# Optimization experiments

Hardware: AMD Instinct MI355X
Metric: run time of the kernel (lower is better)

## Reference

```python
import jax, jax.numpy as jnp
import numpy as np

B, N, C, H = 1, 4096, 512, 8
S = 64  # sqrt(N), static


def setup_inputs() -> dict:
    key = jax.random.key(0)
    ks = jax.random.split(key, 4)
    d = C // H
    return {
        "x": jax.random.normal(ks[0], (B, N, C), dtype=jnp.float32),
        "num_heads": H,
        "bias": jnp.zeros((1,), dtype=jnp.float32),  # unused in original forward
        "scale": jnp.asarray(d ** -0.5, dtype=jnp.float32),
        "Wqkv": jax.random.normal(ks[1], (3 * C, C), dtype=jnp.float32) * (C ** -0.5),
        "bqkv": jnp.zeros((3 * C,), dtype=jnp.float32),
        "Wproj": jax.random.normal(ks[2], (C, C), dtype=jnp.float32) * (C ** -0.5),
        "bproj": jnp.zeros((C,), dtype=jnp.float32),
    }


def reference(x, num_heads, bias, scale, Wqkv, bqkv, Wproj, bproj):
    b, n, c = x.shape
    d = c // num_heads
    # fused QKV projection: [b, n, 3c] -> [3, b, h, n, d]
    qkv = (x @ Wqkv.T + bqkv).reshape(b, n, 3, num_heads, d).transpose(2, 0, 3, 1, 4)
    q, k, v = qkv[0] * scale, qkv[1], qkv[2]
    attn = jax.nn.softmax(jnp.einsum("bhnd,bhmd->bhnm", q, k), axis=-1)
    out = jnp.einsum("bhnm,bhmd->bhnd", attn, v)
    out = out.transpose(0, 2, 1, 3).reshape(b, n, c)
    out = out @ Wproj.T + bproj
    return out.reshape(b, S, S, c)
```

## Files before the change

### kernel.cpp

```cpp
#include <hip/hip_runtime.h>
#include <stdint.h>

#define NTOK 4096
#define CDIM 512
#define HEADS 8
#define DHEAD 64
#define PHEAD (NTOK * DHEAD)

typedef __bf16 bf16x8 __attribute__((ext_vector_type(8)));
typedef float f32x4 __attribute__((ext_vector_type(4)));

typedef const __attribute__((address_space(1))) unsigned int* gas_ptr;
typedef __attribute__((address_space(3))) unsigned int* las_ptr;

__device__ __forceinline__ unsigned short bfbits(float f) {
    return __builtin_bit_cast(unsigned short, (__bf16)f);
}

__device__ __forceinline__ f32x4 mfma32(bf16x8 a, bf16x8 b, f32x4 c) {
    return __builtin_amdgcn_mfma_f32_16x16x32_bf16(a, b, c, 0, 0, 0);
}

__device__ __forceinline__ void gload16(const unsigned short* g, unsigned short* l) {
    __builtin_amdgcn_global_load_lds((gas_ptr)g, (las_ptr)l, 16, 0, 0);
}

__device__ __forceinline__ void cvt_store8(unsigned short* dst, float4 v0, float4 v1) {
    unsigned short o[8];
    o[0] = bfbits(v0.x); o[1] = bfbits(v0.y); o[2] = bfbits(v0.z); o[3] = bfbits(v0.w);
    o[4] = bfbits(v1.x); o[5] = bfbits(v1.y); o[6] = bfbits(v1.z); o[7] = bfbits(v1.w);
    *(uint4*)dst = *(const uint4*)o;
}

__global__ __launch_bounds__(256) void cast3_k(
    const float* __restrict__ x, const float* __restrict__ wq, const float* __restrict__ wp,
    unsigned short* __restrict__ xb, unsigned short* __restrict__ wqb,
    unsigned short* __restrict__ wpb)
{
    const int b = blockIdx.x;
    const float* src; unsigned short* dst; int off;
    if (b < 1024)      { src = x;  dst = xb;  off = b; }
    else if (b < 1408) { src = wq; dst = wqb; off = b - 1024; }
    else               { src = wp; dst = wpb; off = b - 1408; }
    const int i = (off * 256 + threadIdx.x) * 8;
    const float4 v0 = *(const float4*)(src + i);
    const float4 v1 = *(const float4*)(src + i + 4);
    cvt_store8(dst + i, v0, v1);
}

__global__ __launch_bounds__(256) void gemm_qkv(
    const unsigned short* __restrict__ A,
    const unsigned short* __restrict__ Bm,
    const float* __restrict__ bias,
    const float* __restrict__ scale_p,
    unsigned short* __restrict__ qkv_out)
{
    __shared__ __align__(16) unsigned short smem[64 * 136];
    unsigned short* lA = smem;
    unsigned short* lB = smem + 2048;

    const int tid = threadIdx.x;
    const int mBase = blockIdx.y * 64, nBase = blockIdx.x * 128;
    const int lane = tid & 63;
    const int w = __builtin_amdgcn_readfirstlane(tid >> 6);
    const int l16 = lane & 15, quad = lane >> 4;

    const unsigned short* gA  = &A[(size_t)(mBase + (tid >> 2)) * CDIM + (tid & 3) * 8];
    const unsigned short* gB0 = &Bm[(size_t)(nBase + (tid >> 2)) * CDIM + (tid & 3) * 8];
    const unsigned short* gB1 = &Bm[(size_t)(nBase + 64 + (tid >> 2)) * CDIM + (tid & 3) * 8];
    unsigned short* sA  = &lA[tid * 8];
    unsigned short* sB0 = &lB[tid * 8];
    unsigned short* sB1 = &lB[2048 + tid * 8];

    f32x4 acc[4][2] = {};

    for (int kt = 0; kt < CDIM; kt += 32) {
        __syncthreads();
        gload16(gA + kt, sA);
        gload16(gB0 + kt, sB0);
        gload16(gB1 + kt, sB1);
        __syncthreads();

        bf16x8 af[4], bfr[2];
#pragma unroll
        for (int i = 0; i < 4; ++i)
            af[i] = *(const bf16x8*)&lA[(i * 16 + l16) * 32 + quad * 8];
#pragma unroll
        for (int j = 0; j < 2; ++j)
            bfr[j] = *(const bf16x8*)&lB[(w * 32 + j * 16 + l16) * 32 + quad * 8];
#pragma unroll
        for (int i = 0; i < 4; ++i)
#pragma unroll
            for (int j = 0; j < 2; ++j)
                acc[i][j] = mfma32(af[i], bfr[j], acc[i][j]);
    }

    const int three = nBase >> 9;
    const float scl = scale_p[0] * 1.44269504f;
    const float mul = (three == 0) ? scl : 1.0f;

    __syncthreads();
#pragma unroll
    for (int i = 0; i < 4; ++i)
#pragma unroll
        for (int j = 0; j < 2; ++j)
#pragma unroll
            for (int r = 0; r < 4; ++r) {
                const int rl = i * 16 + quad * 4 + r;
                const int cl = w * 32 + j * 16 + l16;
                const float v = (acc[i][j][r] + bias[nBase + cl]) * mul;
                smem[rl * 136 + cl] = bfbits(v);
            }
    __syncthreads();

    const size_t base3 = (size_t)three * (PHEAD * HEADS);
    if (three < 2) {
#pragma unroll
        for (int pass = 0; pass < 4; ++pass) {
            const int idx = pass * 256 + tid;
            const int rl16 = idx & 15, qc = (idx >> 4) & 7;
            const int hsel = (idx >> 7) & 1, t16l = (idx >> 8) & 3;
            const uint4 d = *(const uint4*)&smem[(t16l * 16 + rl16) * 136 + hsel * 64 + qc * 8];
            const int hh = ((nBase >> 6) + hsel) & 7;
            const int t16 = (mBase >> 4) + t16l;
            const size_t dst = base3 + (size_t)hh * PHEAD +
                (size_t)(((t16 * 2 + (qc >> 2)) * 64 + (qc & 3) * 16 + rl16) * 8);
            *(uint4*)&qkv_out[dst] = d;
        }
    } else {
#pragma unroll
        for (int pass = 0; pass < 4; ++pass) {
            const int idx = pass * 256 + tid;
            const int l16t = idx & 15, quadt = (idx >> 4) & 3;
            const int dt = (idx >> 6) & 3, k32l = (idx >> 8) & 1, hsel = (idx >> 9) & 1;
            const int col = hsel * 64 + dt * 16 + l16t;
            unsigned short o8[8];
#pragma unroll
            for (int e = 0; e < 4; ++e) {
                o8[e]     = smem[(k32l * 32 + quadt * 4 + e) * 136 + col];
                o8[e + 4] = smem[(k32l * 32 + 16 + quadt * 4 + e) * 136 + col];
            }
            const int hh = ((nBase >> 6) + hsel) & 7;
            const int k32 = (mBase >> 5) + k32l;
            const size_t dst = base3 + (size_t)hh * PHEAD +
                (size_t)(((k32 * 4 + dt) * 64 + quadt * 16 + l16t) * 8);
            *(uint4*)&qkv_out[dst] = *(uint4*)o8;
        }
    }
}

__global__ __launch_bounds__(256, 2) void flash8_k(
    const unsigned short* __restrict__ qf,
    const unsigned short* __restrict__ kf,
    const unsigned short* __restrict__ vf,
    unsigned short* __restrict__ attn_out)
{
    __shared__ float ldsO[4][64][68];
    __shared__ float sml[4][64];

    const int tid = threadIdx.x;
    const int lane = tid & 63;
    const int w = __builtin_amdgcn_readfirstlane(tid >> 6);
    const int l16 = lane & 15, quad = lane >> 4;
    const int h = blockIdx.x, qb = blockIdx.y;

    const unsigned short* qh = qf + (size_t)h * PHEAD;
    const unsigned short* kb = kf + (size_t)h * PHEAD + w * 65536;
    const unsigned short* vb = vf + (size_t)h * PHEAD + w * 65536;

    bf16x8 qfr[4][2];
#pragma unroll
    for (int qt = 0; qt < 4; ++qt)
#pragma unroll
        for (int d2 = 0; d2 < 2; ++d2)
            qfr[qt][d2] = *(const bf16x8*)&qh[((qb * 4 + qt) * 2 + d2) * 512 + lane * 8];

    f32x4 oacc[4][4] = {};
    float lv[4] = {};

    bf16x8 kA[4], kB[4], vA[4], vB[4];
#pragma unroll
    for (int i = 0; i < 4; ++i) {
        kA[i] = *(const bf16x8*)&kb[i * 512 + lane * 8];
        vA[i] = *(const bf16x8*)&vb[i * 512 + lane * 8];
    }

    auto body = [&](int g, bf16x8* kuse, bf16x8* kload, bf16x8* vuse, bf16x8* vload) {
        const int gn = (g + 1) & 31;
#pragma unroll
        for (int i = 0; i < 4; ++i)
            kload[i] = *(const bf16x8*)&kb[gn * 2048 + i * 512 + lane * 8];
#pragma unroll
        for (int i = 0; i < 4; ++i)
            vload[i] = *(const bf16x8*)&vb[gn * 2048 + i * 512 + lane * 8];

        f32x4 s0[4], s1[4];
        __builtin_amdgcn_s_setprio(1);
#pragma unroll
        for (int qt = 0; qt < 4; ++qt) {
            f32x4 a = {};
            a = mfma32(kuse[0], qfr[qt][0], a);
            a = mfma32(kuse[1], qfr[qt][1], a);
            s0[qt] = a;
            f32x4 b = {};
            b = mfma32(kuse[2], qfr[qt][0], b);
            b = mfma32(kuse[3], qfr[qt][1], b);
            s1[qt] = b;
        }
        __builtin_amdgcn_s_setprio(0);

        bf16x8 pf[4];
#pragma unroll
        for (int qt = 0; qt < 4; ++qt) {
            float e0[4], e1[4];
#pragma unroll
            for (int r = 0; r < 4; ++r) {
                e0[r] = __builtin_amdgcn_exp2f(s0[qt][r]);
                e1[r] = __builtin_amdgcn_exp2f(s1[qt][r]);
            }
            lv[qt] += ((e0[0] + e0[1]) + (e0[2] + e0[3])) +
                      ((e1[0] + e1[1]) + (e1[2] + e1[3]));
            bf16x8 pb;
#pragma unroll
            for (int r = 0; r < 4; ++r) {
                pb[r]     = (__bf16)e0[r];
                pb[4 + r] = (__bf16)e1[r];
            }
            pf[qt] = pb;
        }

        __builtin_amdgcn_s_setprio(1);
#pragma unroll
        for (int dt = 0; dt < 4; ++dt)
#pragma unroll
            for (int qt = 0; qt < 4; ++qt)
                oacc[dt][qt] = mfma32(vuse[dt], pf[qt], oacc[dt][qt]);
        __builtin_amdgcn_s_setprio(0);
    };

    for (int it = 0; it < 16; ++it) {
        body(it * 2 + 0, kA, kB, vA, vB);
        body(it * 2 + 1, kB, kA, vB, vA);
    }

#pragma unroll
    for (int qt = 0; qt < 4; ++qt) {
        float L = lv[qt];
        L += __shfl_xor(L, 16, 64);
        L += __shfl_xor(L, 32, 64);
        if (quad == 0) sml[w][qt * 16 + l16] = L;
    }
#pragma unroll
    for (int qt = 0; qt < 4; ++qt) {
        const int q = qt * 16 + l16;
#pragma unroll
        for (int dt = 0; dt < 4; ++dt)
            *(f32x4*)&ldsO[w][q][dt * 16 + quad * 4] = oacc[dt][qt];
    }
    __syncthreads();
#pragma unroll
    for (int pass = 0; pass < 2; ++pass) {
        const int idx = pass * 256 + tid;
        const int q = idx >> 3, dseg = (idx & 7) * 8;
        const float L = sml[0][q] + sml[1][q] + sml[2][q] + sml[3][q];
        const float inv = 1.f / L;
        unsigned short o8[8];
#pragma unroll
        for (int i = 0; i < 8; ++i) {
            const float v = ldsO[0][q][dseg + i] + ldsO[1][q][dseg + i] +
                            ldsO[2][q][dseg + i] + ldsO[3][q][dseg + i];
            o8[i] = bfbits(v * inv);
        }
        *(uint4*)&attn_out[(size_t)(qb * 64 + q) * CDIM + h * DHEAD + dseg] = *(uint4*)o8;
    }
}

__global__ __launch_bounds__(256) void gemm_proj(
    const unsigned short* __restrict__ A,
    const unsigned short* __restrict__ Bm,
    const float* __restrict__ bias,
    float* __restrict__ c_out)
{
    __shared__ __align__(16) unsigned short smem[2 * 64 * 32];
    unsigned short* lA = smem;
    unsigned short* lB = smem + 2048;

    const int tid = threadIdx.x;
    const int mBase = blockIdx.y * 64, nBase = blockIdx.x * 64;
    const int lane = tid & 63;
    const int w = __builtin_amdgcn_readfirstlane(tid >> 6);
    const int l16 = lane & 15, quad = lane >> 4;

    const unsigned short* gA = &A[(size_t)(mBase + (tid >> 2)) * CDIM + (tid & 3) * 8];
    const unsigned short* gB = &Bm[(size_t)(nBase + (tid >> 2)) * CDIM + (tid & 3) * 8];
    unsigned short* sA = &lA[tid * 8];
    unsigned short* sB = &lB[tid * 8];

    f32x4 acc[4] = {};

    for (int kt = 0; kt < CDIM; kt += 32) {
        __syncthreads();
        gload16(gA + kt, sA);
        gload16(gB + kt, sB);
        __syncthreads();

        bf16x8 af[4], bfr;
#pragma unroll
        for (int i = 0; i < 4; ++i)
            af[i] = *(const bf16x8*)&lA[(i * 16 + l16) * 32 + quad * 8];
        bfr = *(const bf16x8*)&lB[(w * 16 + l16) * 32 + quad * 8];
#pragma unroll
        for (int i = 0; i < 4; ++i)
            acc[i] = mfma32(af[i], bfr, acc[i]);
    }

#pragma unroll
    for (int i = 0; i < 4; ++i)
#pragma unroll
        for (int r = 0; r < 4; ++r) {
            const int grow = mBase + i * 16 + quad * 4 + r;
            const int gcol = nBase + w * 16 + l16;
            c_out[(size_t)grow * CDIM + gcol] = acc[i][r] + bias[gcol];
        }
}

extern "C" void kernel_launch(void* const* d_in, const int* in_sizes, int n_in,
                              void* d_out, int out_size, void* d_ws, size_t ws_size,
                              hipStream_t stream) {
    const float* x       = (const float*)d_in[0];
    const float* scale_p = (const float*)d_in[3];
    const float* Wqkv    = (const float*)d_in[4];
    const float* bqkv    = (const float*)d_in[5];
    const float* Wproj   = (const float*)d_in[6];
    const float* bproj   = (const float*)d_in[7];
    float* out = (float*)d_out;

    char* ws = (char*)d_ws;
    const size_t OFF_QKV  = 0;
    const size_t OFF_ATTN = 12582912;
    const size_t OFF_XB   = 16777216;
    const size_t OFF_WQB  = 20971520;
    const size_t OFF_WPB  = 22544384;
    const size_t NEEDED   = OFF_WPB + 524288;
    if (ws_size < NEEDED) return;

    unsigned short* qkvb  = (unsigned short*)(ws + OFF_QKV);
    unsigned short* attnb = (unsigned short*)(ws + OFF_ATTN);
    unsigned short* xb    = (unsigned short*)(ws + OFF_XB);
    unsigned short* wqb   = (unsigned short*)(ws + OFF_WQB);
    unsigned short* wpb   = (unsigned short*)(ws + OFF_WPB);

    cast3_k<<<1536, 256, 0, stream>>>(x, Wqkv, Wproj, xb, wqb, wpb);

    gemm_qkv<<<dim3(12, 64), 256, 0, stream>>>(xb, wqb, bqkv, scale_p, qkvb);

    const unsigned short* qfr = qkvb;
    const unsigned short* kfr = qkvb + (size_t)PHEAD * HEADS;
    const unsigned short* vfr = qkvb + (size_t)2 * PHEAD * HEADS;
    flash8_k<<<dim3(8, 64), 256, 0, stream>>>(qfr, kfr, vfr, attnb);

    gemm_proj<<<dim3(8, 64), 256, 0, stream>>>(attnb, wpb, bproj, out);
}
```

Measured before the change: 133.0 us.

## Split attention keys across eight waves with 512-thread blocks

The flash attention kernel now uses 512 threads (8 waves), so each wave handles 512 keys instead of 1024 and runs 16 iterations instead of 32. V is no longer double-buffered in registers; it is loaded inside the same iteration it is used, which cuts register use to allow the higher occupancy bound. The cross-wave reduction is chunked into four 16-query passes through a smaller LDS buffer, with syncs in each pass. The risk is exposed V load latency and more barriers and LDS traffic in the epilogue in exchange for more parallel waves.

```diff
diff --git a/kernel.cpp b/kernel.cpp
--- a/kernel.cpp
+++ b/kernel.cpp
@@ -149,14 +149,14 @@
     }
 }
 
-__global__ __launch_bounds__(256, 2) void flash8_k(
+__global__ __launch_bounds__(512, 4) void flash9_k(
     const unsigned short* __restrict__ qf,
     const unsigned short* __restrict__ kf,
     const unsigned short* __restrict__ vf,
     unsigned short* __restrict__ attn_out)
 {
-    __shared__ float ldsO[4][64][68];
-    __shared__ float sml[4][64];
+    __shared__ float ldsO[8][16][68];
+    __shared__ float sml[8][64];
 
     const int tid = threadIdx.x;
     const int lane = tid & 63;
@@ -165,8 +165,8 @@
     const int h = blockIdx.x, qb = blockIdx.y;
 
     const unsigned short* qh = qf + (size_t)h * PHEAD;
-    const unsigned short* kb = kf + (size_t)h * PHEAD + w * 65536;
-    const unsigned short* vb = vf + (size_t)h * PHEAD + w * 65536;
+    const unsigned short* kb = kf + (size_t)h * PHEAD + w * 32768;
+    const unsigned short* vb = vf + (size_t)h * PHEAD + w * 32768;
 
     bf16x8 qfr[4][2];
 #pragma unroll
@@ -178,21 +178,20 @@
     f32x4 oacc[4][4] = {};
     float lv[4] = {};
 
-    bf16x8 kA[4], kB[4], vA[4], vB[4];
-#pragma unroll
-    for (int i = 0; i < 4; ++i) {
+    bf16x8 kA[4], kB[4];
+#pragma unroll
+    for (int i = 0; i < 4; ++i)
         kA[i] = *(const bf16x8*)&kb[i * 512 + lane * 8];
-        vA[i] = *(const bf16x8*)&vb[i * 512 + lane * 8];
-    }
-
-    auto body = [&](int g, bf16x8* kuse, bf16x8* kload, bf16x8* vuse, bf16x8* vload) {
-        const int gn = (g + 1) & 31;
+
+    auto body = [&](int g, bf16x8* kuse, bf16x8* kload) {
+        const int gn = (g + 1) & 15;
 #pragma unroll
         for (int i = 0; i < 4; ++i)
             kload[i] = *(const bf16x8*)&kb[gn * 2048 + i * 512 + lane * 8];
-#pragma unroll
-        for (int i = 0; i < 4; ++i)
-            vload[i] = *(const bf16x8*)&vb[gn * 2048 + i * 512 + lane * 8];
+        bf16x8 vc[4];
+#pragma unroll
+        for (int i = 0; i < 4; ++i)
+            vc[i] = *(const bf16x8*)&vb[g * 2048 + i * 512 + lane * 8];
 
         f32x4 s0[4], s1[4];
         __builtin_amdgcn_s_setprio(1);
@@ -234,13 +233,13 @@
         for (int dt = 0; dt < 4; ++dt)
 #pragma unroll
             for (int qt = 0; qt < 4; ++qt)
-                oacc[dt][qt] = mfma32(vuse[dt], pf[qt], oacc[dt][qt]);
+                oacc[dt][qt] = mfma32(vc[dt], pf[qt], oacc[dt][qt]);
         __builtin_amdgcn_s_setprio(0);
     };
 
-    for (int it = 0; it < 16; ++it) {
-        body(it * 2 + 0, kA, kB, vA, vB);
-        body(it * 2 + 1, kB, kA, vB, vA);
+    for (int it = 0; it < 8; ++it) {
+        body(it * 2 + 0, kA, kB);
+        body(it * 2 + 1, kB, kA);
     }
 
 #pragma unroll
@@ -250,28 +249,31 @@
         L += __shfl_xor(L, 32, 64);
         if (quad == 0) sml[w][qt * 16 + l16] = L;
     }
-#pragma unroll
-    for (int qt = 0; qt < 4; ++qt) {
-        const int q = qt * 16 + l16;
+
+#pragma unroll
+    for (int c = 0; c < 4; ++c) {
 #pragma unroll
         for (int dt = 0; dt < 4; ++dt)
-            *(f32x4*)&ldsO[w][q][dt * 16 + quad * 4] = oacc[dt][qt];
-    }
-    __syncthreads();
-#pragma unroll
-    for (int pass = 0; pass < 2; ++pass) {
-        const int idx = pass * 256 + tid;
-        const int q = idx >> 3, dseg = (idx & 7) * 8;
-        const float L = sml[0][q] + sml[1][q] + sml[2][q] + sml[3][q];
-        const float inv = 1.f / L;
-        unsigned short o8[8];
-#pragma unroll
-        for (int i = 0; i < 8; ++i) {
-            const float v = ldsO[0][q][dseg + i] + ldsO[1][q][dseg + i] +
-                            ldsO[2][q][dseg + i] + ldsO[3][q][dseg + i];
-            o8[i] = bfbits(v * inv);
-        }
-        *(uint4*)&attn_out[(size_t)(qb * 64 + q) * CDIM + h * DHEAD + dseg] = *(uint4*)o8;
+            *(f32x4*)&ldsO[w][l16][dt * 16 + quad * 4] = oacc[dt][c];
+        __syncthreads();
+        {
+            const int ql = tid >> 5, dp = (tid & 31) * 2;
+            const int q = c * 16 + ql;
+            float L = 0.f, v0 = 0.f, v1 = 0.f;
+#pragma unroll
+            for (int ww = 0; ww < 8; ++ww) {
+                L  += sml[ww][q];
+                v0 += ldsO[ww][ql][dp];
+                v1 += ldsO[ww][ql][dp + 1];
+            }
+            const float inv = 1.f / L;
+            unsigned short o2[2];
+            o2[0] = bfbits(v0 * inv);
+            o2[1] = bfbits(v1 * inv);
+            *(unsigned int*)&attn_out[(size_t)(qb * 64 + q) * CDIM + h * DHEAD + dp] =
+                *(const unsigned int*)o2;
+        }
+        __syncthreads();
     }
 }
 
@@ -357,7 +359,7 @@
     const unsigned short* qfr = qkvb;
     const unsigned short* kfr = qkvb + (size_t)PHEAD * HEADS;
     const unsigned short* vfr = qkvb + (size_t)2 * PHEAD * HEADS;
-    flash8_k<<<dim3(8, 64), 256, 0, stream>>>(qfr, kfr, vfr, attnb);
+    flash9_k<<<dim3(8, 64), 512, 0, stream>>>(qfr, kfr, vfr, attnb);
 
     gemm_proj<<<dim3(8, 64), 256, 0, stream>>>(attnb, wpb, bproj, out);
 }
```

Result: slower. 385.7 us (+189.9%).

## Double-buffer LDS in both GEMMs and software-pipeline QK with PV in attention

Applied to the files above, without the earlier changes.

Both GEMM kernels move to two LDS stages: the next K-slice is prefetched with global_load_lds while the current one is consumed, which drops one barrier per iteration. The attention kernel is rebuilt as an explicit software pipeline. The QK^T MFMAs for tile i+1 are issued together with the PV MFMAs for tile i, and K/V register loads are staggered one tile ahead. The aim is to hide exp/softmax and load latency behind matrix work, at the cost of more registers, which may hurt occupancy under the 2-blocks-per-SIMD launch bound.

```diff
diff --git a/kernel.cpp b/kernel.cpp
--- a/kernel.cpp
+++ b/kernel.cpp
@@ -55,9 +55,7 @@
     const float* __restrict__ scale_p,
     unsigned short* __restrict__ qkv_out)
 {
-    __shared__ __align__(16) unsigned short smem[64 * 136];
-    unsigned short* lA = smem;
-    unsigned short* lB = smem + 2048;
+    __shared__ __align__(16) unsigned short smem[2 * 6144];
 
     const int tid = threadIdx.x;
     const int mBase = blockIdx.y * 64, nBase = blockIdx.x * 128;
@@ -68,18 +66,24 @@
     const unsigned short* gA  = &A[(size_t)(mBase + (tid >> 2)) * CDIM + (tid & 3) * 8];
     const unsigned short* gB0 = &Bm[(size_t)(nBase + (tid >> 2)) * CDIM + (tid & 3) * 8];
     const unsigned short* gB1 = &Bm[(size_t)(nBase + 64 + (tid >> 2)) * CDIM + (tid & 3) * 8];
-    unsigned short* sA  = &lA[tid * 8];
-    unsigned short* sB0 = &lB[tid * 8];
-    unsigned short* sB1 = &lB[2048 + tid * 8];
 
     f32x4 acc[4][2] = {};
 
+    gload16(gA, &smem[tid * 8]);
+    gload16(gB0, &smem[2048 + tid * 8]);
+    gload16(gB1, &smem[4096 + tid * 8]);
+
+    int cur = 0;
     for (int kt = 0; kt < CDIM; kt += 32) {
         __syncthreads();
-        gload16(gA + kt, sA);
-        gload16(gB0 + kt, sB0);
-        gload16(gB1 + kt, sB1);
-        __syncthreads();
+        if (kt + 32 < CDIM) {
+            const int nb = (cur ^ 1) * 6144;
+            gload16(gA + kt + 32, &smem[nb + tid * 8]);
+            gload16(gB0 + kt + 32, &smem[nb + 2048 + tid * 8]);
+            gload16(gB1 + kt + 32, &smem[nb + 4096 + tid * 8]);
+        }
+        const unsigned short* lA = &smem[cur * 6144];
+        const unsigned short* lB = &smem[cur * 6144 + 2048];
 
         bf16x8 af[4], bfr[2];
 #pragma unroll
@@ -93,6 +97,7 @@
 #pragma unroll
             for (int j = 0; j < 2; ++j)
                 acc[i][j] = mfma32(af[i], bfr[j], acc[i][j]);
+        cur ^= 1;
     }
 
     const int three = nBase >> 9;
@@ -149,7 +154,7 @@
     }
 }
 
-__global__ __launch_bounds__(256, 2) void flash8_k(
+__global__ __launch_bounds__(256, 2) void flash10_k(
     const unsigned short* __restrict__ qf,
     const unsigned short* __restrict__ kf,
     const unsigned short* __restrict__ vf,
@@ -178,45 +183,41 @@
     f32x4 oacc[4][4] = {};
     float lv[4] = {};
 
-    bf16x8 kA[4], kB[4], vA[4], vB[4];
-#pragma unroll
-    for (int i = 0; i < 4; ++i) {
-        kA[i] = *(const bf16x8*)&kb[i * 512 + lane * 8];
-        vA[i] = *(const bf16x8*)&vb[i * 512 + lane * 8];
-    }
-
-    auto body = [&](int g, bf16x8* kuse, bf16x8* kload, bf16x8* vuse, bf16x8* vload) {
-        const int gn = (g + 1) & 31;
-#pragma unroll
-        for (int i = 0; i < 4; ++i)
-            kload[i] = *(const bf16x8*)&kb[gn * 2048 + i * 512 + lane * 8];
-#pragma unroll
-        for (int i = 0; i < 4; ++i)
-            vload[i] = *(const bf16x8*)&vb[gn * 2048 + i * 512 + lane * 8];
-
-        f32x4 s0[4], s1[4];
-        __builtin_amdgcn_s_setprio(1);
+    bf16x8 k0[4], k1[4], v0[4], v1[4];
+    f32x4 s[4][2];
+    bf16x8 pf[4];
+
+    auto LK = [&](bf16x8* dst, int t) {
+#pragma unroll
+        for (int i = 0; i < 4; ++i)
+            dst[i] = *(const bf16x8*)&kb[t * 2048 + i * 512 + lane * 8];
+    };
+    auto LV = [&](bf16x8* dst, int t) {
+#pragma unroll
+        for (int i = 0; i < 4; ++i)
+            dst[i] = *(const bf16x8*)&vb[t * 2048 + i * 512 + lane * 8];
+    };
+    auto QK = [&](bf16x8* ku) {
 #pragma unroll
         for (int qt = 0; qt < 4; ++qt) {
             f32x4 a = {};
-            a = mfma32(kuse[0], qfr[qt][0], a);
-            a = mfma32(kuse[1], qfr[qt][1], a);
-            s0[qt] = a;
+            a = mfma32(ku[0], qfr[qt][0], a);
+            a = mfma32(ku[1], qfr[qt][1], a);
+            s[qt][0] = a;
             f32x4 b = {};
-            b = mfma32(kuse[2], qfr[qt][0], b);
-            b = mfma32(kuse[3], qfr[qt][1], b);
-            s1[qt] = b;
-        }
-        __builtin_amdgcn_s_setprio(0);
-
-        bf16x8 pf[4];
+            b = mfma32(ku[2], qfr[qt][0], b);
+            b = mfma32(ku[3], qfr[qt][1], b);
+            s[qt][1] = b;
+        }
+    };
+    auto SM = [&]() {
 #pragma unroll
         for (int qt = 0; qt < 4; ++qt) {
             float e0[4], e1[4];
 #pragma unroll
             for (int r = 0; r < 4; ++r) {
-                e0[r] = __builtin_amdgcn_exp2f(s0[qt][r]);
-                e1[r] = __builtin_amdgcn_exp2f(s1[qt][r]);
+                e0[r] = __builtin_amdgcn_exp2f(s[qt][0][r]);
+                e1[r] = __builtin_amdgcn_exp2f(s[qt][1][r]);
             }
             lv[qt] += ((e0[0] + e0[1]) + (e0[2] + e0[3])) +
                       ((e1[0] + e1[1]) + (e1[2] + e1[3]));
@@ -228,20 +229,43 @@
             }
             pf[qt] = pb;
         }
-
+    };
+    auto PV = [&](bf16x8* vu) {
+#pragma unroll
+        for (int dt = 0; dt < 4; ++dt)
+#pragma unroll
+            for (int qt = 0; qt < 4; ++qt)
+                oacc[dt][qt] = mfma32(vu[dt], pf[qt], oacc[dt][qt]);
+    };
+
+    LK(k0, 0); LV(v0, 0); LK(k1, 1);
+    QK(k0);
+
+    for (int ii = 0; ii < 15; ++ii) {
+        const int i = ii * 2 + 1;
+        LK(k0, i + 1);
+        LV(v1, i);
+        SM();
         __builtin_amdgcn_s_setprio(1);
-#pragma unroll
-        for (int dt = 0; dt < 4; ++dt)
-#pragma unroll
-            for (int qt = 0; qt < 4; ++qt)
-                oacc[dt][qt] = mfma32(vuse[dt], pf[qt], oacc[dt][qt]);
+        QK(k1);
+        PV(v0);
         __builtin_amdgcn_s_setprio(0);
-    };
-
-    for (int it = 0; it < 16; ++it) {
-        body(it * 2 + 0, kA, kB, vA, vB);
-        body(it * 2 + 1, kB, kA, vB, vA);
-    }
+        LK(k1, i + 2);
+        LV(v0, i + 1);
+        SM();
+        __builtin_amdgcn_s_setprio(1);
+        QK(k0);
+        PV(v1);
+        __builtin_amdgcn_s_setprio(0);
+    }
+    LV(v1, 31);
+    SM();
+    __builtin_amdgcn_s_setprio(1);
+    QK(k1);
+    PV(v0);
+    __builtin_amdgcn_s_setprio(0);
+    SM();
+    PV(v1);
 
 #pragma unroll
     for (int qt = 0; qt < 4; ++qt) {
@@ -281,9 +305,7 @@
     const float* __restrict__ bias,
     float* __restrict__ c_out)
 {
-    __shared__ __align__(16) unsigned short smem[2 * 64 * 32];
-    unsigned short* lA = smem;
-    unsigned short* lB = smem + 2048;
+    __shared__ __align__(16) unsigned short smem[2 * 4096];
 
     const int tid = threadIdx.x;
     const int mBase = blockIdx.y * 64, nBase = blockIdx.x * 64;
@@ -293,16 +315,22 @@
 
     const unsigned short* gA = &A[(size_t)(mBase + (tid >> 2)) * CDIM + (tid & 3) * 8];
     const unsigned short* gB = &Bm[(size_t)(nBase + (tid >> 2)) * CDIM + (tid & 3) * 8];
-    unsigned short* sA = &lA[tid * 8];
-    unsigned short* sB = &lB[tid * 8];
 
     f32x4 acc[4] = {};
 
+    gload16(gA, &smem[tid * 8]);
+    gload16(gB, &smem[2048 + tid * 8]);
+
+    int cur = 0;
     for (int kt = 0; kt < CDIM; kt += 32) {
         __syncthreads();
-        gload16(gA + kt, sA);
-        gload16(gB + kt, sB);
-        __syncthreads();
+        if (kt + 32 < CDIM) {
+            const int nb = (cur ^ 1) * 4096;
+            gload16(gA + kt + 32, &smem[nb + tid * 8]);
+            gload16(gB + kt + 32, &smem[nb + 2048 + tid * 8]);
+        }
+        const unsigned short* lA = &smem[cur * 4096];
+        const unsigned short* lB = &smem[cur * 4096 + 2048];
 
         bf16x8 af[4], bfr;
 #pragma unroll
@@ -312,6 +340,7 @@
 #pragma unroll
         for (int i = 0; i < 4; ++i)
             acc[i] = mfma32(af[i], bfr, acc[i]);
+        cur ^= 1;
     }
 
 #pragma unroll
@@ -357,7 +386,7 @@
     const unsigned short* qfr = qkvb;
     const unsigned short* kfr = qkvb + (size_t)PHEAD * HEADS;
     const unsigned short* vfr = qkvb + (size_t)2 * PHEAD * HEADS;
-    flash8_k<<<dim3(8, 64), 256, 0, stream>>>(qfr, kfr, vfr, attnb);
+    flash10_k<<<dim3(8, 64), 256, 0, stream>>>(qfr, kfr, vfr, attnb);
 
     gemm_proj<<<dim3(8, 64), 256, 0, stream>>>(attnb, wpb, bproj, out);
 }
```

Result: slower. 147.9 us (+11.2%).

## Double-buffer LDS tiles and XOR-swizzle layout in QKV and projection GEMMs

Applied to the files above, without the earlier changes.

Both GEMM kernels now use two LDS buffers: the next K-slice is prefetched with global_load_lds while MFMAs run on the current one. This drops one barrier per iteration. The 16-byte chunks are also XOR-swizzled by row when loaded, and un-swizzled when reading fragments, to reduce LDS bank conflicts. The cost is twice the LDS per block, which may lower occupancy. The barrier likely still waits on the outstanding prefetch, which limits how much load and compute actually overlap.

```diff
diff --git a/kernel.cpp b/kernel.cpp
--- a/kernel.cpp
+++ b/kernel.cpp
@@ -55,9 +55,7 @@
     const float* __restrict__ scale_p,
     unsigned short* __restrict__ qkv_out)
 {
-    __shared__ __align__(16) unsigned short smem[64 * 136];
-    unsigned short* lA = smem;
-    unsigned short* lB = smem + 2048;
+    __shared__ __align__(16) unsigned short smem[2 * 6144];
 
     const int tid = threadIdx.x;
     const int mBase = blockIdx.y * 64, nBase = blockIdx.x * 128;
@@ -65,34 +63,45 @@
     const int w = __builtin_amdgcn_readfirstlane(tid >> 6);
     const int l16 = lane & 15, quad = lane >> 4;
 
-    const unsigned short* gA  = &A[(size_t)(mBase + (tid >> 2)) * CDIM + (tid & 3) * 8];
-    const unsigned short* gB0 = &Bm[(size_t)(nBase + (tid >> 2)) * CDIM + (tid & 3) * 8];
-    const unsigned short* gB1 = &Bm[(size_t)(nBase + 64 + (tid >> 2)) * CDIM + (tid & 3) * 8];
-    unsigned short* sA  = &lA[tid * 8];
-    unsigned short* sB0 = &lB[tid * 8];
-    unsigned short* sB1 = &lB[2048 + tid * 8];
+    const int srow = tid >> 2;
+    const int scol = ((tid & 3) ^ ((tid >> 3) & 3)) * 8;
+    const unsigned short* gA  = &A[(size_t)(mBase + srow) * CDIM + scol];
+    const unsigned short* gB0 = &Bm[(size_t)(nBase + srow) * CDIM + scol];
+    const unsigned short* gB1 = &Bm[(size_t)(nBase + 64 + srow) * CDIM + scol];
+
+    const int qs = (quad ^ ((l16 >> 1) & 3)) * 8;
 
     f32x4 acc[4][2] = {};
 
+    gload16(gA, &smem[tid * 8]);
+    gload16(gB0, &smem[2048 + tid * 8]);
+    gload16(gB1, &smem[4096 + tid * 8]);
+
+    int cur = 0;
     for (int kt = 0; kt < CDIM; kt += 32) {
         __syncthreads();
-        gload16(gA + kt, sA);
-        gload16(gB0 + kt, sB0);
-        gload16(gB1 + kt, sB1);
-        __syncthreads();
+        if (kt + 32 < CDIM) {
+            const int nb = (cur ^ 1) * 6144;
+            gload16(gA + kt + 32, &smem[nb + tid * 8]);
+            gload16(gB0 + kt + 32, &smem[nb + 2048 + tid * 8]);
+            gload16(gB1 + kt + 32, &smem[nb + 4096 + tid * 8]);
+        }
+        const unsigned short* lA = &smem[cur * 6144];
+        const unsigned short* lB = &smem[cur * 6144 + 2048];
 
         bf16x8 af[4], bfr[2];
 #pragma unroll
         for (int i = 0; i < 4; ++i)
-            af[i] = *(const bf16x8*)&lA[(i * 16 + l16) * 32 + quad * 8];
+            af[i] = *(const bf16x8*)&lA[(i * 16 + l16) * 32 + qs];
 #pragma unroll
         for (int j = 0; j < 2; ++j)
-            bfr[j] = *(const bf16x8*)&lB[(w * 32 + j * 16 + l16) * 32 + quad * 8];
+            bfr[j] = *(const bf16x8*)&lB[(w * 32 + j * 16 + l16) * 32 + qs];
 #pragma unroll
         for (int i = 0; i < 4; ++i)
 #pragma unroll
             for (int j = 0; j < 2; ++j)
                 acc[i][j] = mfma32(af[i], bfr[j], acc[i][j]);
+        cur ^= 1;
     }
 
     const int three = nBase >> 9;
@@ -281,9 +290,7 @@
     const float* __restrict__ bias,
     float* __restrict__ c_out)
 {
-    __shared__ __align__(16) unsigned short smem[2 * 64 * 32];
-    unsigned short* lA = smem;
-    unsigned short* lB = smem + 2048;
+    __shared__ __align__(16) unsigned short smem[2 * 4096];
 
     const int tid = threadIdx.x;
     const int mBase = blockIdx.y * 64, nBase = blockIdx.x * 64;
@@ -291,27 +298,38 @@
     const int w = __builtin_amdgcn_readfirstlane(tid >> 6);
     const int l16 = lane & 15, quad = lane >> 4;
 
-    const unsigned short* gA = &A[(size_t)(mBase + (tid >> 2)) * CDIM + (tid & 3) * 8];
-    const unsigned short* gB = &Bm[(size_t)(nBase + (tid >> 2)) * CDIM + (tid & 3) * 8];
-    unsigned short* sA = &lA[tid * 8];
-    unsigned short* sB = &lB[tid * 8];
+    const int srow = tid >> 2;
+    const int scol = ((tid & 3) ^ ((tid >> 3) & 3)) * 8;
+    const unsigned short* gA = &A[(size_t)(mBase + srow) * CDIM + scol];
+    const unsigned short* gB = &Bm[(size_t)(nBase + srow) * CDIM + scol];
+
+    const int qs = (quad ^ ((l16 >> 1) & 3)) * 8;
 
     f32x4 acc[4] = {};
 
+    gload16(gA, &smem[tid * 8]);
+    gload16(gB, &smem[2048 + tid * 8]);
+
+    int cur = 0;
     for (int kt = 0; kt < CDIM; kt += 32) {
         __syncthreads();
-        gload16(gA + kt, sA);
-        gload16(gB + kt, sB);
-        __syncthreads();
+        if (kt + 32 < CDIM) {
+            const int nb = (cur ^ 1) * 4096;
+            gload16(gA + kt + 32, &smem[nb + tid * 8]);
+            gload16(gB + kt + 32, &smem[nb + 2048 + tid * 8]);
+        }
+        const unsigned short* lA = &smem[cur * 4096];
+        const unsigned short* lB = &smem[cur * 4096 + 2048];
 
         bf16x8 af[4], bfr;
 #pragma unroll
         for (int i = 0; i < 4; ++i)
-            af[i] = *(const bf16x8*)&lA[(i * 16 + l16) * 32 + quad * 8];
-        bfr = *(const bf16x8*)&lB[(w * 16 + l16) * 32 + quad * 8];
+            af[i] = *(const bf16x8*)&lA[(i * 16 + l16) * 32 + qs];
+        bfr = *(const bf16x8*)&lB[(w * 16 + l16) * 32 + qs];
 #pragma unroll
         for (int i = 0; i < 4; ++i)
             acc[i] = mfma32(af[i], bfr, acc[i]);
+        cur ^= 1;
     }
 
 #pragma unroll
```

After: 131.4 us. No clear change (-1.2%).
